# Optimization experiments

Measured on AMD Instinct MI355X. Metric: run time of the kernel, lower is better.

The kernel has to match this reference:

```python
import jax, jax.numpy as jnp
import numpy as np

N, K = 16384, 25
D_SELF, D_NEIGH, D_LINK, D_OUT = 256, 256, 64, 256


def _glorot(key, shape):
    fan = shape[0] if len(shape) == 1 else (shape[0] + shape[1])
    limit = np.sqrt(6.0 / fan).astype(np.float32)
    return jax.random.uniform(key, shape, jnp.float32, -limit, limit)


def setup_inputs() -> dict:
    key = jax.random.key(0)
    ks = jax.random.split(key, 10)
    return {
        "self_vecs": jax.random.normal(ks[0], (N, D_SELF), jnp.float32),
        "neigh_vecs": jax.random.normal(ks[1], (N, K, D_NEIGH), jnp.float32),
        "link_vecs": jax.random.normal(ks[2], (N, K, D_LINK), jnp.float32),
        # keep probs away from 0 to avoid huge 1/p values
        "select_probs": jax.random.uniform(ks[3], (N, K), jnp.float32) * 0.9 + 0.1,
        # Gate parameters (weight vectors)
        "g_self_w": _glorot(ks[4], (D_SELF,)),
        "g_neigh_w": _glorot(ks[5], (D_NEIGH,)),
        "g_link_w": _glorot(ks[6], (D_LINK,)),
        # Aggregator parameters
        "W_link": _glorot(ks[7], (D_LINK, D_NEIGH)),
        "W_self": _glorot(ks[8], (D_SELF, D_OUT)),
        "W_neigh": _glorot(ks[9], (D_NEIGH, D_OUT)),
    }


def reference(self_vecs, neigh_vecs, link_vecs, select_probs,
              g_self_w, g_neigh_w, g_link_w, W_link, W_self, W_neigh):
    # dropout = 0.0 -> identity
    # Gate: sigmoid(trans_self[:, None] + trans_neigh + trans_link)  -> [N, K]
    trans_self = self_vecs @ g_self_w                                  # [N]
    trans_neigh = jnp.einsum('nkd,d->nk', neigh_vecs, g_neigh_w)       # [N, K]
    trans_link = jnp.einsum('nkl,l->nk', link_vecs, g_link_w)          # [N, K]
    gate = jax.nn.sigmoid(trans_self[:, None] + trans_neigh + trans_link)

    # link-conditioned amplification of neighbor features
    trans_links = jax.nn.sigmoid(jnp.einsum('nkl,ld->nkd', link_vecs, W_link))  # [N, K, D_NEIGH]
    amplified = neigh_vecs * trans_links

    # select_probs provided -> gate/prob weighting and mean over neighbors
    w = gate / select_probs                                            # [N, K]
    expected = jnp.mean(amplified * w[..., None], axis=-2)             # [N, D_NEIGH]

    from_self = self_vecs @ W_self                                     # [N, D_OUT]
    from_neighs = expected @ W_neigh                                   # [N, D_OUT]
    out = jnp.concatenate([from_self, from_neighs], axis=-1)           # concat combination
    return jax.nn.relu(out)
```

## Files before the change

### kernel.cpp

```cpp
#include <hip/hip_runtime.h>

#define DEV __device__ __forceinline__

typedef __bf16 bf16;
typedef bf16 bf16x4 __attribute__((ext_vector_type(4)));
typedef bf16 bf16x8 __attribute__((ext_vector_type(8)));
typedef float f32x4 __attribute__((ext_vector_type(4)));

constexpr int N_NODES = 16384;
constexpr int KN = 25;
constexpr int DS = 256, DN = 256, DL = 64;

constexpr size_t WS_WLT  = 0;
constexpr size_t WS_WCAT = 32768;
constexpr size_t WS_EXP  = 32768 + 262144;

DEV float sigmoid_fast(float x) {
    return __builtin_amdgcn_rcpf(1.0f + __builtin_amdgcn_exp2f(-1.44269504088896341f * x));
}

DEV float dot4(f32x4 a, f32x4 b) {
    return a[0] * b[0] + a[1] * b[1] + a[2] * b[2] + a[3] * b[3];
}

__global__ void prep_kernel(const float* __restrict__ W_link,
                            const float* __restrict__ W_self,
                            const float* __restrict__ W_neigh,
                            bf16* __restrict__ wlT, bf16* __restrict__ wcat) {
    int tid = blockIdx.x * blockDim.x + threadIdx.x;
    int stride = gridDim.x * blockDim.x;
    for (int i = tid; i < DL * DN; i += stride) {
        int d = i >> 6, l = i & 63;
        wlT[i] = (bf16)W_link[l * DN + d];
    }
    for (int i = tid; i < 512 * 256; i += stride) {
        int j = i >> 8, kk = i & 255;
        float v = (j < 256) ? W_self[kk * 256 + j] : W_neigh[kk * 256 + (j - 256)];
        wcat[i] = (bf16)v;
    }
}

constexpr int NPW = 8;
constexpr int WTS = 72;
constexpr int STS = 264;

__global__ __launch_bounds__(256, 2)
void fused_agg_kernel(const float* __restrict__ self_vecs,
                      const float* __restrict__ neigh_vecs,
                      const float* __restrict__ link_vecs,
                      const float* __restrict__ probs,
                      const float* __restrict__ g_self_w,
                      const float* __restrict__ g_neigh_w,
                      const float* __restrict__ g_link_w,
                      const bf16* __restrict__ wlT,
                      bf16* __restrict__ exp_out) {
    __shared__ bf16 WT[256 * WTS];
    __shared__ bf16 ST[4][16 * STS];

    const int tid = threadIdx.x;
    const int lane = tid & 63;
    const int w = tid >> 6;
    const int c = lane & 15;
    const int q = lane >> 4;

    for (int i = 0; i < 16; ++i) {
        int idx = i * 1024 + tid * 4;
        int d = idx >> 6, l = idx & 63;
        *(bf16x4*)&WT[d * WTS + l] = *(const bf16x4*)&wlT[idx];
    }
    __syncthreads();

    f32x4 gsw = *(const f32x4*)&g_self_w[lane * 4];
    f32x4 gnw = *(const f32x4*)&g_neigh_w[lane * 4];
    f32x4 glw0a = *(const f32x4*)&g_link_w[q * 8];
    f32x4 glw0b = *(const f32x4*)&g_link_w[q * 8 + 4];
    f32x4 glw1a = *(const f32x4*)&g_link_w[32 + q * 8];
    f32x4 glw1b = *(const f32x4*)&g_link_w[32 + q * 8 + 4];

    for (int it = 0; it < NPW; ++it) {
        const int n = (blockIdx.x * 4 + w) * NPW + it;
        const float* nbase = neigh_vecs + (size_t)n * KN * DN;
        const float* lbase = link_vecs + (size_t)n * KN * DL;

        f32x4 sv = *(const f32x4*)&self_vecs[(size_t)n * DS + lane * 4];
        float ts = dot4(sv, gsw);
#pragma unroll
        for (int off = 1; off < 64; off <<= 1) ts += __shfl_xor(ts, off);

        f32x4 v0 = *(const f32x4*)&lbase[c * DL + q * 8];
        f32x4 v1 = *(const f32x4*)&lbase[c * DL + q * 8 + 4];
        f32x4 v2 = *(const f32x4*)&lbase[c * DL + 32 + q * 8];
        f32x4 v3 = *(const f32x4*)&lbase[c * DL + 32 + q * 8 + 4];
        const int rB = c + 16;
        const f32x4 z = {0.f, 0.f, 0.f, 0.f};
        f32x4 u0 = z, u1 = z, u2 = z, u3 = z;
        if (rB < KN) {
            u0 = *(const f32x4*)&lbase[rB * DL + q * 8];
            u1 = *(const f32x4*)&lbase[rB * DL + q * 8 + 4];
            u2 = *(const f32x4*)&lbase[rB * DL + 32 + q * 8];
            u3 = *(const f32x4*)&lbase[rB * DL + 32 + q * 8 + 4];
        }
        bf16x8 a00, a01, a10, a11;
#pragma unroll
        for (int j = 0; j < 4; ++j) {
            a00[j] = (bf16)v0[j]; a00[j + 4] = (bf16)v1[j];
            a01[j] = (bf16)v2[j]; a01[j + 4] = (bf16)v3[j];
            a10[j] = (bf16)u0[j]; a10[j + 4] = (bf16)u1[j];
            a11[j] = (bf16)u2[j]; a11[j + 4] = (bf16)u3[j];
        }
        float tlA = dot4(v0, glw0a) + dot4(v1, glw0b) + dot4(v2, glw1a) + dot4(v3, glw1b);
        tlA += __shfl_xor(tlA, 16); tlA += __shfl_xor(tlA, 32);
        float tlB = dot4(u0, glw0a) + dot4(u1, glw0b) + dot4(u2, glw1a) + dot4(u3, glw1b);
        tlB += __shfl_xor(tlB, 16); tlB += __shfl_xor(tlB, 32);

        float gk = ts + ((lane & 63) < 16 ? tlA : tlB);
        float pv = (lane < KN) ? probs[n * KN + lane] : 1.0f;
        float wden = __builtin_amdgcn_rcpf(pv * 25.0f);

        f32x4 accd = z;

#pragma unroll
        for (int half = 0; half < 2; ++half) {
            const bf16x8 aF0 = half ? a10 : a00;
            const bf16x8 aF1 = half ? a11 : a01;
            const int k0 = half * 16;
            const int kcnt = half ? (KN - 16) : 16;

            f32x4 nv[16];
#pragma unroll
            for (int kk = 0; kk < 16; ++kk) {
                if (kk < kcnt)
                    nv[kk] = *(const f32x4*)&nbase[(size_t)(k0 + kk) * DN + lane * 4];
            }

#pragma unroll
            for (int t = 0; t < 16; ++t) {
                bf16x8 b0 = *(const bf16x8*)&WT[(t * 16 + c) * WTS + q * 8];
                bf16x8 b1 = *(const bf16x8*)&WT[(t * 16 + c) * WTS + 32 + q * 8];
                f32x4 acc = z;
                acc = __builtin_amdgcn_mfma_f32_16x16x32_bf16(aF0, b0, acc, 0, 0, 0);
                acc = __builtin_amdgcn_mfma_f32_16x16x32_bf16(aF1, b1, acc, 0, 0, 0);
#pragma unroll
                for (int r = 0; r < 4; ++r)
                    ST[w][(q * 4 + r) * STS + t * 16 + c] = (bf16)sigmoid_fast(acc[r]);
            }

#pragma unroll
            for (int kk = 0; kk < kcnt; ++kk) {
                const int k = k0 + kk;
                f32x4 nvk = nv[kk];
                bf16x4 s4 = *(const bf16x4*)&ST[w][kk * STS + lane * 4];
                float tn = dot4(nvk, gnw);
#pragma unroll
                for (int off = 1; off < 64; off <<= 1) tn += __shfl_xor(tn, off);
                float wkk = sigmoid_fast(tn + __shfl(gk, k)) * __shfl(wden, k);
#pragma unroll
                for (int j = 0; j < 4; ++j)
                    accd[j] += nvk[j] * (float)s4[j] * wkk;
            }
        }

        bf16x4 eo;
#pragma unroll
        for (int j = 0; j < 4; ++j) eo[j] = (bf16)accd[j];
        *(bf16x4*)&exp_out[(size_t)n * DN + lane * 4] = eo;
    }
}

constexpr int BPAD = 72;

__global__ __launch_bounds__(256, 2)
void out_gemm_kernel(const float* __restrict__ self_vecs,
                     const bf16* __restrict__ exp_in,
                     const bf16* __restrict__ wcat,
                     float* __restrict__ out) {
    __shared__ bf16 As[64 * BPAD];
    __shared__ bf16 Bs[64 * BPAD];
    const int tid = threadIdx.x;
    const int lane = tid & 63;
    const int w = tid >> 6;
    const int c = lane & 15, q = lane >> 4;
    const int wm = w >> 1, wn = w & 1;
    const int m0 = blockIdx.x * 64;
    const int j0 = blockIdx.y * 64;
    const bool use_exp = j0 >= 256;

    f32x4 acc[2][2];
#pragma unroll
    for (int i = 0; i < 2; ++i)
#pragma unroll
        for (int j = 0; j < 2; ++j) acc[i][j] = (f32x4){0.f, 0.f, 0.f, 0.f};

    const int srow = tid >> 4;
    const int scol = (tid & 15) * 4;

    for (int ks = 0; ks < 4; ++ks) {
        const int k0 = ks * 64;
        __syncthreads();
#pragma unroll
        for (int i = 0; i < 4; ++i) {
            int row = srow + i * 16;
            if (use_exp) {
                *(bf16x4*)&As[row * BPAD + scol] =
                    *(const bf16x4*)&exp_in[(size_t)(m0 + row) * 256 + k0 + scol];
            } else {
                f32x4 v = *(const f32x4*)&self_vecs[(size_t)(m0 + row) * 256 + k0 + scol];
                bf16x4 b; b[0] = (bf16)v[0]; b[1] = (bf16)v[1]; b[2] = (bf16)v[2]; b[3] = (bf16)v[3];
                *(bf16x4*)&As[row * BPAD + scol] = b;
            }
            *(bf16x4*)&Bs[row * BPAD + scol] =
                *(const bf16x4*)&wcat[(size_t)(j0 + row) * 256 + k0 + scol];
        }
        __syncthreads();
        const int kc = q * 8;
#pragma unroll
        for (int i = 0; i < 2; ++i) {
            bf16x8 a0 = *(const bf16x8*)&As[(wm * 32 + i * 16 + c) * BPAD + kc];
            bf16x8 a1 = *(const bf16x8*)&As[(wm * 32 + i * 16 + c) * BPAD + kc + 32];
#pragma unroll
            for (int j = 0; j < 2; ++j) {
                bf16x8 b0 = *(const bf16x8*)&Bs[(wn * 32 + j * 16 + c) * BPAD + kc];
                bf16x8 b1 = *(const bf16x8*)&Bs[(wn * 32 + j * 16 + c) * BPAD + kc + 32];
                acc[i][j] = __builtin_amdgcn_mfma_f32_16x16x32_bf16(a0, b0, acc[i][j], 0, 0, 0);
                acc[i][j] = __builtin_amdgcn_mfma_f32_16x16x32_bf16(a1, b1, acc[i][j], 0, 0, 0);
            }
        }
    }

#pragma unroll
    for (int i = 0; i < 2; ++i)
#pragma unroll
        for (int j = 0; j < 2; ++j)
#pragma unroll
            for (int r = 0; r < 4; ++r) {
                int row = m0 + wm * 32 + i * 16 + q * 4 + r;
                int col = j0 + wn * 32 + j * 16 + c;
                float v = acc[i][j][r];
                out[(size_t)row * 512 + col] = v > 0.f ? v : 0.f;
            }
}

extern "C" void kernel_launch(void* const* d_in, const int* in_sizes, int n_in,
                              void* d_out, int out_size, void* d_ws, size_t ws_size,
                              hipStream_t stream) {
    const float* self_vecs  = (const float*)d_in[0];
    const float* neigh_vecs = (const float*)d_in[1];
    const float* link_vecs  = (const float*)d_in[2];
    const float* probs      = (const float*)d_in[3];
    const float* g_self_w   = (const float*)d_in[4];
    const float* g_neigh_w  = (const float*)d_in[5];
    const float* g_link_w   = (const float*)d_in[6];
    const float* W_link     = (const float*)d_in[7];
    const float* W_self     = (const float*)d_in[8];
    const float* W_neigh    = (const float*)d_in[9];
    float* out = (float*)d_out;

    char* ws = (char*)d_ws;
    bf16* wlT  = (bf16*)(ws + WS_WLT);
    bf16* wcat = (bf16*)(ws + WS_WCAT);
    bf16* expb = (bf16*)(ws + WS_EXP);

    prep_kernel<<<dim3(128), dim3(256), 0, stream>>>(W_link, W_self, W_neigh, wlT, wcat);
    fused_agg_kernel<<<dim3(N_NODES / (4 * NPW)), dim3(256), 0, stream>>>(
        self_vecs, neigh_vecs, link_vecs, probs, g_self_w, g_neigh_w, g_link_w, wlT, expb);
    out_gemm_kernel<<<dim3(256, 8), dim3(256), 0, stream>>>(self_vecs, expb, wcat, out);
}
```

Measured before the change: 676.9 us.

## Prefetch next node's link/self/prob data and widen output GEMM tile to 256 columns

In the aggregation kernel, the self vector, link vectors and selection probs for the next node are loaded into registers while the current node is processed, hiding their load latency behind the neighbor work. The output GEMM now computes a 64x256 tile per block (grid 256x2 instead of 256x8). This reuses each A tile across all 256 columns and avoids redundant fp32-to-bf16 conversion of self_vecs. The wider tile raises register and LDS use (8 accumulators per row group, a 256-row B buffer), which may lower occupancy.

```diff
diff --git a/kernel.cpp b/kernel.cpp
--- a/kernel.cpp
+++ b/kernel.cpp
@@ -77,29 +77,37 @@
     f32x4 glw1a = *(const f32x4*)&g_link_w[32 + q * 8];
     f32x4 glw1b = *(const f32x4*)&g_link_w[32 + q * 8 + 4];
 
+    const int rB = c + 16;
+    const f32x4 z = {0.f, 0.f, 0.f, 0.f};
+    const int nfirst = (blockIdx.x * 4 + w) * NPW;
+
+    f32x4 sv, v0, v1, v2, v3, u0, u1, u2, u3;
+    float pvr;
+    {
+        const float* lb = link_vecs + (size_t)nfirst * KN * DL;
+        sv = *(const f32x4*)&self_vecs[(size_t)nfirst * DS + lane * 4];
+        v0 = *(const f32x4*)&lb[c * DL + q * 8];
+        v1 = *(const f32x4*)&lb[c * DL + q * 8 + 4];
+        v2 = *(const f32x4*)&lb[c * DL + 32 + q * 8];
+        v3 = *(const f32x4*)&lb[c * DL + 32 + q * 8 + 4];
+        u0 = z; u1 = z; u2 = z; u3 = z;
+        if (rB < KN) {
+            u0 = *(const f32x4*)&lb[rB * DL + q * 8];
+            u1 = *(const f32x4*)&lb[rB * DL + q * 8 + 4];
+            u2 = *(const f32x4*)&lb[rB * DL + 32 + q * 8];
+            u3 = *(const f32x4*)&lb[rB * DL + 32 + q * 8 + 4];
+        }
+        pvr = (lane < KN) ? probs[(size_t)nfirst * KN + lane] : 1.0f;
+    }
+
     for (int it = 0; it < NPW; ++it) {
-        const int n = (blockIdx.x * 4 + w) * NPW + it;
+        const int n = nfirst + it;
         const float* nbase = neigh_vecs + (size_t)n * KN * DN;
-        const float* lbase = link_vecs + (size_t)n * KN * DL;
-
-        f32x4 sv = *(const f32x4*)&self_vecs[(size_t)n * DS + lane * 4];
+
         float ts = dot4(sv, gsw);
 #pragma unroll
         for (int off = 1; off < 64; off <<= 1) ts += __shfl_xor(ts, off);
 
-        f32x4 v0 = *(const f32x4*)&lbase[c * DL + q * 8];
-        f32x4 v1 = *(const f32x4*)&lbase[c * DL + q * 8 + 4];
-        f32x4 v2 = *(const f32x4*)&lbase[c * DL + 32 + q * 8];
-        f32x4 v3 = *(const f32x4*)&lbase[c * DL + 32 + q * 8 + 4];
-        const int rB = c + 16;
-        const f32x4 z = {0.f, 0.f, 0.f, 0.f};
-        f32x4 u0 = z, u1 = z, u2 = z, u3 = z;
-        if (rB < KN) {
-            u0 = *(const f32x4*)&lbase[rB * DL + q * 8];
-            u1 = *(const f32x4*)&lbase[rB * DL + q * 8 + 4];
-            u2 = *(const f32x4*)&lbase[rB * DL + 32 + q * 8];
-            u3 = *(const f32x4*)&lbase[rB * DL + 32 + q * 8 + 4];
-        }
         bf16x8 a00, a01, a10, a11;
 #pragma unroll
         for (int j = 0; j < 4; ++j) {
@@ -113,9 +121,26 @@
         float tlB = dot4(u0, glw0a) + dot4(u1, glw0b) + dot4(u2, glw1a) + dot4(u3, glw1b);
         tlB += __shfl_xor(tlB, 16); tlB += __shfl_xor(tlB, 32);
 
-        float gk = ts + ((lane & 63) < 16 ? tlA : tlB);
-        float pv = (lane < KN) ? probs[n * KN + lane] : 1.0f;
-        float wden = __builtin_amdgcn_rcpf(pv * 25.0f);
+        float gk = ts + (lane < 16 ? tlA : tlB);
+        float wden = __builtin_amdgcn_rcpf(pvr * 25.0f);
+
+        if (it + 1 < NPW) {
+            const int n2 = n + 1;
+            const float* lb2 = link_vecs + (size_t)n2 * KN * DL;
+            sv = *(const f32x4*)&self_vecs[(size_t)n2 * DS + lane * 4];
+            v0 = *(const f32x4*)&lb2[c * DL + q * 8];
+            v1 = *(const f32x4*)&lb2[c * DL + q * 8 + 4];
+            v2 = *(const f32x4*)&lb2[c * DL + 32 + q * 8];
+            v3 = *(const f32x4*)&lb2[c * DL + 32 + q * 8 + 4];
+            u0 = z; u1 = z; u2 = z; u3 = z;
+            if (rB < KN) {
+                u0 = *(const f32x4*)&lb2[rB * DL + q * 8];
+                u1 = *(const f32x4*)&lb2[rB * DL + q * 8 + 4];
+                u2 = *(const f32x4*)&lb2[rB * DL + 32 + q * 8];
+                u3 = *(const f32x4*)&lb2[rB * DL + 32 + q * 8 + 4];
+            }
+            pvr = (lane < KN) ? probs[(size_t)n2 * KN + lane] : 1.0f;
+        }
 
         f32x4 accd = z;
 
@@ -175,21 +200,22 @@
                      const bf16* __restrict__ wcat,
                      float* __restrict__ out) {
     __shared__ bf16 As[64 * BPAD];
-    __shared__ bf16 Bs[64 * BPAD];
+    __shared__ bf16 Bs[256 * BPAD];
     const int tid = threadIdx.x;
     const int lane = tid & 63;
     const int w = tid >> 6;
     const int c = lane & 15, q = lane >> 4;
-    const int wm = w >> 1, wn = w & 1;
+    const int wm = w >> 1;
+    const int wn = w & 1;
     const int m0 = blockIdx.x * 64;
-    const int j0 = blockIdx.y * 64;
-    const bool use_exp = j0 >= 256;
-
-    f32x4 acc[2][2];
+    const int jbase = blockIdx.y * 256;
+    const bool use_exp = blockIdx.y != 0;
+
+    f32x4 acc[2][8];
 #pragma unroll
     for (int i = 0; i < 2; ++i)
 #pragma unroll
-        for (int j = 0; j < 2; ++j) acc[i][j] = (f32x4){0.f, 0.f, 0.f, 0.f};
+        for (int j = 0; j < 8; ++j) acc[i][j] = (f32x4){0.f, 0.f, 0.f, 0.f};
 
     const int srow = tid >> 4;
     const int scol = (tid & 15) * 4;
@@ -208,8 +234,12 @@
                 bf16x4 b; b[0] = (bf16)v[0]; b[1] = (bf16)v[1]; b[2] = (bf16)v[2]; b[3] = (bf16)v[3];
                 *(bf16x4*)&As[row * BPAD + scol] = b;
             }
+        }
+#pragma unroll
+        for (int i = 0; i < 16; ++i) {
+            int row = srow + i * 16;
             *(bf16x4*)&Bs[row * BPAD + scol] =
-                *(const bf16x4*)&wcat[(size_t)(j0 + row) * 256 + k0 + scol];
+                *(const bf16x4*)&wcat[(size_t)(jbase + row) * 256 + k0 + scol];
         }
         __syncthreads();
         const int kc = q * 8;
@@ -218,9 +248,9 @@
             bf16x8 a0 = *(const bf16x8*)&As[(wm * 32 + i * 16 + c) * BPAD + kc];
             bf16x8 a1 = *(const bf16x8*)&As[(wm * 32 + i * 16 + c) * BPAD + kc + 32];
 #pragma unroll
-            for (int j = 0; j < 2; ++j) {
-                bf16x8 b0 = *(const bf16x8*)&Bs[(wn * 32 + j * 16 + c) * BPAD + kc];
-                bf16x8 b1 = *(const bf16x8*)&Bs[(wn * 32 + j * 16 + c) * BPAD + kc + 32];
+            for (int j = 0; j < 8; ++j) {
+                bf16x8 b0 = *(const bf16x8*)&Bs[(wn * 128 + j * 16 + c) * BPAD + kc];
+                bf16x8 b1 = *(const bf16x8*)&Bs[(wn * 128 + j * 16 + c) * BPAD + kc + 32];
                 acc[i][j] = __builtin_amdgcn_mfma_f32_16x16x32_bf16(a0, b0, acc[i][j], 0, 0, 0);
                 acc[i][j] = __builtin_amdgcn_mfma_f32_16x16x32_bf16(a1, b1, acc[i][j], 0, 0, 0);
             }
@@ -230,11 +260,11 @@
 #pragma unroll
     for (int i = 0; i < 2; ++i)
 #pragma unroll
-        for (int j = 0; j < 2; ++j)
+        for (int j = 0; j < 8; ++j)
 #pragma unroll
             for (int r = 0; r < 4; ++r) {
                 int row = m0 + wm * 32 + i * 16 + q * 4 + r;
-                int col = j0 + wn * 32 + j * 16 + c;
+                int col = jbase + wn * 128 + j * 16 + c;
                 float v = acc[i][j][r];
                 out[(size_t)row * 512 + col] = v > 0.f ? v : 0.f;
             }
@@ -263,5 +293,5 @@
     prep_kernel<<<dim3(128), dim3(256), 0, stream>>>(W_link, W_self, W_neigh, wlT, wcat);
     fused_agg_kernel<<<dim3(N_NODES / (4 * NPW)), dim3(256), 0, stream>>>(
         self_vecs, neigh_vecs, link_vecs, probs, g_self_w, g_neigh_w, g_link_w, wlT, expb);
-    out_gemm_kernel<<<dim3(256, 8), dim3(256), 0, stream>>>(self_vecs, expb, wcat, out);
-}
+    out_gemm_kernel<<<dim3(256, 2), dim3(256), 0, stream>>>(self_vecs, expb, wcat, out);
+}
```

Result: no change. 675.4 us (-0.2%).
